# Optimization experiments

Hardware: AMD Instinct MI355X
Metric: run time of the kernel (lower is better)

Reference implementation:

```python
import jax, jax.numpy as jnp
import numpy as np

S1, S2, S3 = 2, 16, 1  # hardcoded layer sizes from __init__


def _lstm_cell(x, h, c, w_ih, w_hh, b_ih, b_hh):
    # torch.nn.LSTMCell gate order: i, f, g, o
    gates = x @ w_ih.T + b_ih + h @ w_hh.T + b_hh
    i, f, g, o = jnp.split(gates, 4, axis=-1)
    i = jax.nn.sigmoid(i)
    f = jax.nn.sigmoid(f)
    g = jnp.tanh(g)
    o = jax.nn.sigmoid(o)
    c_new = f * c + i * g
    h_new = o * jnp.tanh(c_new)
    return h_new, c_new


def setup_inputs() -> dict:
    key = jax.random.key(0)
    ks = jax.random.split(key, 16)
    B, T = 16384, 2048
    x = jax.random.normal(ks[0], (B, T * S1), dtype=jnp.float32)

    def u(k, shape, fan):
        bound = 1.0 / np.sqrt(fan)
        return jax.random.uniform(k, shape, jnp.float32, -bound, bound)

    return {
        "x": x,
        # lstm1: LSTMCell(2, 2)
        "w_ih1": u(ks[1], (4 * S1, S1), S1), "w_hh1": u(ks[2], (4 * S1, S1), S1),
        "b_ih1": u(ks[3], (4 * S1,), S1),   "b_hh1": u(ks[4], (4 * S1,), S1),
        # lstm2: LSTMCell(2, 16)
        "w_ih2": u(ks[5], (4 * S2, S1), S2), "w_hh2": u(ks[6], (4 * S2, S2), S2),
        "b_ih2": u(ks[7], (4 * S2,), S2),   "b_hh2": u(ks[8], (4 * S2,), S2),
        # lstm3: LSTMCell(16, 1)
        "w_ih3": u(ks[9], (4 * S3, S2), S3), "w_hh3": u(ks[10], (4 * S3, S3), S3),
        "b_ih3": u(ks[11], (4 * S3,), S3),  "b_hh3": u(ks[12], (4 * S3,), S3),
        # linear: Linear(1, 1)
        "w_lin": u(ks[13], (S3, S3), S3), "b_lin": u(ks[14], (S3,), S3),
    }


def reference(x, w_ih1, w_hh1, b_ih1, b_hh1,
              w_ih2, w_hh2, b_ih2, b_hh2,
              w_ih3, w_hh3, b_ih3, b_hh3,
              w_lin, b_lin):
    B = x.shape[0]
    T = x.shape[1] // S1
    # [B, T*2] -> [T, B, 2] (time-major for scan)
    xt = x.reshape(B, T, S1).transpose(1, 0, 2)

    h1 = jnp.zeros((B, S1), x.dtype); c1 = jnp.zeros((B, S1), x.dtype)
    h2 = jnp.zeros((B, S2), x.dtype); c2 = jnp.zeros((B, S2), x.dtype)
    h3 = jnp.zeros((B, S3), x.dtype); c3 = jnp.zeros((B, S3), x.dtype)

    def step(carry, x_t):
        h1, c1, h2, c2, h3, c3 = carry
        h1, c1 = _lstm_cell(x_t, h1, c1, w_ih1, w_hh1, b_ih1, b_hh1)
        h2, c2 = _lstm_cell(h1, h2, c2, w_ih2, w_hh2, b_ih2, b_hh2)
        h3, c3 = _lstm_cell(h2, h3, c3, w_ih3, w_hh3, b_ih3, b_hh3)
        out = h3 @ w_lin.T + b_lin  # [B, 1]
        return (h1, c1, h2, c2, h3, c3), out

    _, ys = jax.lax.scan(step, (h1, c1, h2, c2, h3, c3), xt)
    # ys: [T, B, 1] -> cat along dim=1 of per-step [B,1] outputs -> [B, T]
    return ys[:, :, 0].T
```

## Files before the change

kernel.cpp:

```cpp
#include <hip/hip_runtime.h>

typedef _Float16 f16x8 __attribute__((ext_vector_type(8)));
typedef float    f32x4 __attribute__((ext_vector_type(4)));
typedef unsigned u32x4 __attribute__((ext_vector_type(4)));

#define DEV __device__ __forceinline__

DEV float fexp2(float x){ return __builtin_amdgcn_exp2f(x); }
DEV float frcp (float x){ return __builtin_amdgcn_rcpf(x); }

DEV float sgm(float p){ return frcp(1.0f + fexp2(p)); }
DEV float tnc(float c){ return fmaf(2.f, sgm(c * -2.88539008177792682f), -1.f); }

DEV float shx(float v, int m){ return __shfl_xor(v, m, 64); }

DEV unsigned pkrne(float a, float b){
  unsigned short ha = __builtin_bit_cast(unsigned short, (_Float16)a);
  unsigned short hb = __builtin_bit_cast(unsigned short, (_Float16)b);
  return (unsigned)ha | ((unsigned)hb << 16);
}

#define L2E_N  (-1.44269504088896341f)
#define L2E2_N (-2.88539008177792682f)

__global__ __launch_bounds__(256, 1)
void lstm3_kernel(const float* __restrict__ x,
                  const float* __restrict__ w_ih1, const float* __restrict__ w_hh1,
                  const float* __restrict__ b_ih1, const float* __restrict__ b_hh1,
                  const float* __restrict__ w_ih2, const float* __restrict__ w_hh2,
                  const float* __restrict__ b_ih2, const float* __restrict__ b_hh2,
                  const float* __restrict__ w_ih3, const float* __restrict__ w_hh3,
                  const float* __restrict__ b_ih3, const float* __restrict__ b_hh3,
                  const float* __restrict__ w_lin, const float* __restrict__ b_lin,
                  float* __restrict__ out, int T)
{
  const int tid = threadIdx.x;
  const int l   = tid & 63;
  const int n   = l & 15;
  const int g   = l >> 4;
  const int wv  = tid >> 6;
  const int seq = 16 * (blockIdx.x * 4 + wv) + n;

  const int rA = g, rB = 4 + g;
  const float sAq = L2E_N;
  const float sBq = (g < 2) ? L2E2_N : L2E_N;
  const float m1  = (g < 2) ? 2.0f : 1.0f;
  const float a1  = (g < 2) ? -1.0f : 0.0f;
  const float w1ax = w_ih1[2*rA]*sAq,  w1ay = w_ih1[2*rA+1]*sAq;
  const float w1ah0 = w_hh1[2*rA]*sAq, w1ah1 = w_hh1[2*rA+1]*sAq;
  const float bbA  = (b_ih1[rA] + b_hh1[rA]) * sAq;
  const float w1bx = w_ih1[2*rB]*sBq,  w1by = w_ih1[2*rB+1]*sBq;
  const float w1bh0 = w_hh1[2*rB]*sBq, w1bh1 = w_hh1[2*rB+1]*sBq;
  const float bbB  = (b_ih1[rB] + b_hh1[rB]) * sBq;

  f16x8 af[4];
  f16x8 a2f[4];
  f32x4 cb[4];
  #pragma unroll
  for (int t = 0; t < 4; ++t){
    const float sc = (t == 2) ? L2E2_N : L2E_N;
    #pragma unroll
    for (int e = 0; e < 8; ++e){
      float v = 0.0f;
      if (e < 4) v = w_hh2[(16*t + n)*16 + (4*g + e)];
      af[t][e] = (_Float16)(v * sc);
      float v2 = 0.0f;
      if (g == 0 && e < 2) v2 = w_ih2[(16*t + n)*2 + e];
      a2f[t][e] = (_Float16)(v2 * sc);
    }
    #pragma unroll
    for (int j = 0; j < 4; ++j){
      const int r = 16*t + 4*g + j;
      cb[t][j] = (b_ih2[r] + b_hh2[r]) * sc;
    }
  }

  const float s3n = ((n & 3) == 2) ? L2E2_N : L2E_N;
  f16x8 a3f;
  #pragma unroll
  for (int e = 0; e < 8; ++e){
    float v = 0.0f;
    if (e < 4) v = w_ih3[16*(n & 3) + 4*g + e] * s3n;
    a3f[e] = (_Float16)v;
  }
  f32x4 c3v;
  c3v[0] = (b_ih3[0] + b_hh3[0]) * L2E_N;
  c3v[1] = (b_ih3[1] + b_hh3[1]) * L2E_N;
  c3v[2] = (b_ih3[2] + b_hh3[2]) * L2E2_N;
  c3v[3] = (b_ih3[3] + b_hh3[3]) * L2E_N;
  const float wh30 = w_hh3[0] * L2E_N,  wh31 = w_hh3[1] * L2E_N;
  const float wh32 = w_hh3[2] * L2E2_N, wh33 = w_hh3[3] * L2E_N;
  const float wl = w_lin[0], bl = b_lin[0];

  float c1 = 0.f, c3 = 0.f;
  float c2[4] = {0.f, 0.f, 0.f, 0.f};
  float h1a_all = 0.f, h1b_all = 0.f, h3 = 0.f;
  unsigned pAu = 0u, pBu = 0u;
  unsigned h1p = 0u;

  const float* xrow = x + (size_t)seq * (size_t)(2*T);
  float*       orow = out + (size_t)seq * (size_t)T;

  float2 x_use = *(const float2*)(xrow);
  float2 x_pre = *(const float2*)(xrow + 2);

  #define LSTM1_STEP(X0, X1)                                                   \
  {                                                                            \
    const float gA = fmaf(w1ax, (X0), fmaf(w1ay, (X1),                         \
                     fmaf(w1ah0, h1a_all, fmaf(w1ah1, h1b_all, bbA))));        \
    const float gB = fmaf(w1bx, (X0), fmaf(w1by, (X1),                         \
                     fmaf(w1bh0, h1a_all, fmaf(w1bh1, h1b_all, bbB))));        \
    const float zA = sgm(gA);                                                  \
    const float zB = fmaf(sgm(gB), m1, a1);                                    \
    const float ig1 = zA * zB;                                                 \
    const float fm = shx(zA, 32);                                              \
    c1 = fmaf(fm, c1, ig1);                                                    \
    const float th1 = tnc(c1);                                                 \
    const float om = shx(zB, 32);                                              \
    const float h1v = om * th1;                                                \
    const float t16 = shx(h1v, 16);                                            \
    h1p = pkrne(h1v, t16);                         \
    const float a_c = (g & 1) ? t16 : h1v;                                     \
    const float b_c = (g & 1) ? h1v : t16;                                     \
    const float a32 = shx(a_c, 32);                                            \
    const float b32 = shx(b_c, 32);                                            \
    h1a_all = (g & 2) ? a32 : a_c;                                             \
    h1b_all = (g & 2) ? b32 : b_c;                                             \
  }

  LSTM1_STEP(x_use.x, x_use.y)

  float o0 = 0.f, o1 = 0.f, o2 = 0.f, o3 = 0.f;

  f32x4 dp0, dp1, dp2, dp3;
  {
    u32x4 bu; bu[0] = 0u; bu[1] = 0u; bu[2] = 0u; bu[3] = 0u;
    const f16x8 bv = __builtin_bit_cast(f16x8, bu);
    dp0 = __builtin_amdgcn_mfma_f32_16x16x32_f16(af[0], bv, cb[0], 0, 0, 0);
    dp1 = __builtin_amdgcn_mfma_f32_16x16x32_f16(af[1], bv, cb[1], 0, 0, 0);
    dp2 = __builtin_amdgcn_mfma_f32_16x16x32_f16(af[2], bv, cb[2], 0, 0, 0);
    dp3 = __builtin_amdgcn_mfma_f32_16x16x32_f16(af[3], bv, cb[3], 0, 0, 0);
  }

  const int NCH = T / 4;
  for (int ch = 0; ch < NCH; ++ch){
    const bool cap = (g == (ch & 3));

    #pragma unroll
    for (int s = 0; s < 4; ++s){
      u32x4 b2u; b2u[0] = (g == 0) ? h1p : 0u; b2u[1] = 0u; b2u[2] = 0u; b2u[3] = 0u;
      const f16x8 b2v = __builtin_bit_cast(f16x8, b2u);
      const f32x4 d0 = __builtin_amdgcn_mfma_f32_16x16x32_f16(a2f[0], b2v, dp0, 0, 0, 0);
      const f32x4 d1 = __builtin_amdgcn_mfma_f32_16x16x32_f16(a2f[1], b2v, dp1, 0, 0, 0);
      const f32x4 d2 = __builtin_amdgcn_mfma_f32_16x16x32_f16(a2f[2], b2v, dp2, 0, 0, 0);
      const f32x4 d3 = __builtin_amdgcn_mfma_f32_16x16x32_f16(a2f[3], b2v, dp3, 0, 0, 0);

      const float2 xv = x_pre;
      const int ti = 4*ch + s + 2;
      const int tc = (ti < T) ? ti : (T - 1);
      x_pre = *(const float2*)(xrow + 2*tc);

      LSTM1_STEP(xv.x, xv.y)

      float h2l[4];
      #pragma unroll
      for (int j = 0; j < 4; ++j){
        const float ii = sgm(d0[j]);
        const float ff = sgm(d1[j]);
        const float gg = fmaf(2.f, sgm(d2[j]), -1.f);
        const float oo = sgm(d3[j]);
        c2[j] = fmaf(ff, c2[j], ii * gg);
        h2l[j] = oo * tnc(c2[j]);
      }
      pAu = pkrne(h2l[0], h2l[1]);
      pBu = pkrne(h2l[2], h2l[3]);

      u32x4 bu; bu[0] = pAu; bu[1] = pBu; bu[2] = 0u; bu[3] = 0u;
      const f16x8 bv = __builtin_bit_cast(f16x8, bu);
      dp0 = __builtin_amdgcn_mfma_f32_16x16x32_f16(af[0], bv, cb[0], 0, 0, 0);
      dp1 = __builtin_amdgcn_mfma_f32_16x16x32_f16(af[1], bv, cb[1], 0, 0, 0);
      dp2 = __builtin_amdgcn_mfma_f32_16x16x32_f16(af[2], bv, cb[2], 0, 0, 0);
      dp3 = __builtin_amdgcn_mfma_f32_16x16x32_f16(af[3], bv, cb[3], 0, 0, 0);

      const f32x4 d3v = __builtin_amdgcn_mfma_f32_16x16x32_f16(a3f, bv, c3v, 0, 0, 0);
      const float p_i = fmaf(wh30, h3, d3v[0]);
      const float p_f = fmaf(wh31, h3, d3v[1]);
      const float p_g = fmaf(wh32, h3, d3v[2]);
      const float p_o = fmaf(wh33, h3, d3v[3]);
      const float i3 = sgm(p_i);
      const float f3 = sgm(p_f);
      const float g3 = fmaf(2.f, sgm(p_g), -1.f);
      const float q3 = sgm(p_o);
      c3 = fmaf(f3, c3, i3 * g3);
      h3 = q3 * tnc(c3);
      const float yv = fmaf(wl, h3, bl);

      if      (s == 0) o0 = cap ? yv : o0;
      else if (s == 1) o1 = cap ? yv : o1;
      else if (s == 2) o2 = cap ? yv : o2;
      else             o3 = cap ? yv : o3;
    }

    if ((ch & 3) == 3){
      float4 o4; o4.x = o0; o4.y = o1; o4.z = o2; o4.w = o3;
      *(float4*)(orow + (ch >> 2) * 16 + 4 * g) = o4;
    }
  }
  #undef LSTM1_STEP
}

extern "C" void kernel_launch(void* const* d_in, const int* in_sizes, int n_in,
                              void* d_out, int out_size, void* d_ws, size_t ws_size,
                              hipStream_t stream)
{
  const float* x     = (const float*)d_in[0];
  const float* w_ih1 = (const float*)d_in[1];
  const float* w_hh1 = (const float*)d_in[2];
  const float* b_ih1 = (const float*)d_in[3];
  const float* b_hh1 = (const float*)d_in[4];
  const float* w_ih2 = (const float*)d_in[5];
  const float* w_hh2 = (const float*)d_in[6];
  const float* b_ih2 = (const float*)d_in[7];
  const float* b_hh2 = (const float*)d_in[8];
  const float* w_ih3 = (const float*)d_in[9];
  const float* w_hh3 = (const float*)d_in[10];
  const float* b_ih3 = (const float*)d_in[11];
  const float* b_hh3 = (const float*)d_in[12];
  const float* w_lin = (const float*)d_in[13];
  const float* b_lin = (const float*)d_in[14];
  float* out = (float*)d_out;

  const int T = 2048;
  const int B = in_sizes[0] / (2 * T);
  const int waves   = B / 16;
  const int blocks  = waves / 4;

  lstm3_kernel<<<blocks, 256, 0, stream>>>(
      x, w_ih1, w_hh1, b_ih1, b_hh1,
      w_ih2, w_hh2, b_ih2, b_hh2,
      w_ih3, w_hh3, b_ih3, b_hh3,
      w_lin, b_lin, out, T);
}
```

Measured before the change: 1.085 ms.

## Split LSTM layers across producer/consumer wave pairs via LDS double buffer

Each group of 16 sequences is now handled by two waves. A producer wave runs LSTM layers 1 and 2 and writes packed h2 into a double-buffered LDS slot, and a consumer wave runs layer 3 plus the linear output one step behind. This shortens each wave's serial dependency chain and doubles the wave count, with launch bounds raised so two blocks can share a CU. The cost is a __syncthreads every timestep and twice the blocks for the same batch. Which wave of the pair produces alternates with block index.

```diff
diff --git a/kernel.cpp b/kernel.cpp
--- a/kernel.cpp
+++ b/kernel.cpp
@@ -23,7 +23,7 @@
 #define L2E_N  (-1.44269504088896341f)
 #define L2E2_N (-2.88539008177792682f)
 
-__global__ __launch_bounds__(256, 1)
+__global__ __launch_bounds__(256, 2)
 void lstm3_kernel(const float* __restrict__ x,
                   const float* __restrict__ w_ih1, const float* __restrict__ w_hh1,
                   const float* __restrict__ b_ih1, const float* __restrict__ b_hh1,
@@ -34,12 +34,17 @@
                   const float* __restrict__ w_lin, const float* __restrict__ b_lin,
                   float* __restrict__ out, int T)
 {
+  __shared__ unsigned long long lbuf[2][2][64];
+
   const int tid = threadIdx.x;
   const int l   = tid & 63;
   const int n   = l & 15;
   const int g   = l >> 4;
   const int wv  = tid >> 6;
-  const int seq = 16 * (blockIdx.x * 4 + wv) + n;
+  const int pr  = wv >> 1;
+  const int par = (blockIdx.x >> 8) & 1;
+  const bool isP = ((wv & 1) == par);
+  const int seq = 16 * (blockIdx.x * 2 + pr) + n;
 
   const int rA = g, rB = 4 + g;
   const float sAq = L2E_N;
@@ -95,7 +100,6 @@
   float c1 = 0.f, c3 = 0.f;
   float c2[4] = {0.f, 0.f, 0.f, 0.f};
   float h1a_all = 0.f, h1b_all = 0.f, h3 = 0.f;
-  unsigned pAu = 0u, pBu = 0u;
   unsigned h1p = 0u;
 
   const float* xrow = x + (size_t)seq * (size_t)(2*T);
@@ -119,7 +123,7 @@
     const float om = shx(zB, 32);                                              \
     const float h1v = om * th1;                                                \
     const float t16 = shx(h1v, 16);                                            \
-    h1p = pkrne(h1v, t16);                         \
+    h1p = pkrne(h1v, t16);                                                     \
     const float a_c = (g & 1) ? t16 : h1v;                                     \
     const float b_c = (g & 1) ? h1v : t16;                                     \
     const float a32 = shx(a_c, 32);                                            \
@@ -129,8 +133,6 @@
   }
 
   LSTM1_STEP(x_use.x, x_use.y)
-
-  float o0 = 0.f, o1 = 0.f, o2 = 0.f, o3 = 0.f;
 
   f32x4 dp0, dp1, dp2, dp3;
   {
@@ -142,12 +144,10 @@
     dp3 = __builtin_amdgcn_mfma_f32_16x16x32_f16(af[3], bv, cb[3], 0, 0, 0);
   }
 
-  const int NCH = T / 4;
-  for (int ch = 0; ch < NCH; ++ch){
-    const bool cap = (g == (ch & 3));
-
-    #pragma unroll
-    for (int s = 0; s < 4; ++s){
+  float o0 = 0.f, o1 = 0.f, o2 = 0.f, o3 = 0.f;
+
+  for (int t = 0; t <= T; ++t){
+    if (isP && t < T){
       u32x4 b2u; b2u[0] = (g == 0) ? h1p : 0u; b2u[1] = 0u; b2u[2] = 0u; b2u[3] = 0u;
       const f16x8 b2v = __builtin_bit_cast(f16x8, b2u);
       const f32x4 d0 = __builtin_amdgcn_mfma_f32_16x16x32_f16(a2f[0], b2v, dp0, 0, 0, 0);
@@ -156,7 +156,7 @@
       const f32x4 d3 = __builtin_amdgcn_mfma_f32_16x16x32_f16(a2f[3], b2v, dp3, 0, 0, 0);
 
       const float2 xv = x_pre;
-      const int ti = 4*ch + s + 2;
+      const int ti = t + 2;
       const int tc = (ti < T) ? ti : (T - 1);
       x_pre = *(const float2*)(xrow + 2*tc);
 
@@ -172,8 +172,8 @@
         c2[j] = fmaf(ff, c2[j], ii * gg);
         h2l[j] = oo * tnc(c2[j]);
       }
-      pAu = pkrne(h2l[0], h2l[1]);
-      pBu = pkrne(h2l[2], h2l[3]);
+      const unsigned pAu = pkrne(h2l[0], h2l[1]);
+      const unsigned pBu = pkrne(h2l[2], h2l[3]);
 
       u32x4 bu; bu[0] = pAu; bu[1] = pBu; bu[2] = 0u; bu[3] = 0u;
       const f16x8 bv = __builtin_bit_cast(f16x8, bu);
@@ -182,6 +182,16 @@
       dp2 = __builtin_amdgcn_mfma_f32_16x16x32_f16(af[2], bv, cb[2], 0, 0, 0);
       dp3 = __builtin_amdgcn_mfma_f32_16x16x32_f16(af[3], bv, cb[3], 0, 0, 0);
 
+      lbuf[pr][t & 1][l] = ((unsigned long long)pBu << 32) | (unsigned long long)pAu;
+    }
+
+    if (!isP && t > 0){
+      const int u = t - 1;
+      const unsigned long long v = lbuf[pr][u & 1][l];
+      const unsigned pAu = (unsigned)v;
+      const unsigned pBu = (unsigned)(v >> 32);
+      u32x4 bu; bu[0] = pAu; bu[1] = pBu; bu[2] = 0u; bu[3] = 0u;
+      const f16x8 bv = __builtin_bit_cast(f16x8, bu);
       const f32x4 d3v = __builtin_amdgcn_mfma_f32_16x16x32_f16(a3f, bv, c3v, 0, 0, 0);
       const float p_i = fmaf(wh30, h3, d3v[0]);
       const float p_f = fmaf(wh31, h3, d3v[1]);
@@ -195,16 +205,21 @@
       h3 = q3 * tnc(c3);
       const float yv = fmaf(wl, h3, bl);
 
+      const int ch = u >> 2;
+      const int s  = u & 3;
+      const bool cap = (g == (ch & 3));
       if      (s == 0) o0 = cap ? yv : o0;
       else if (s == 1) o1 = cap ? yv : o1;
       else if (s == 2) o2 = cap ? yv : o2;
       else             o3 = cap ? yv : o3;
-    }
-
-    if ((ch & 3) == 3){
-      float4 o4; o4.x = o0; o4.y = o1; o4.z = o2; o4.w = o3;
-      *(float4*)(orow + (ch >> 2) * 16 + 4 * g) = o4;
-    }
+
+      if ((u & 15) == 15){
+        float4 o4; o4.x = o0; o4.y = o1; o4.z = o2; o4.w = o3;
+        *(float4*)(orow + (u >> 4) * 16 + 4 * g) = o4;
+      }
+    }
+
+    __syncthreads();
   }
   #undef LSTM1_STEP
 }
@@ -232,8 +247,7 @@
 
   const int T = 2048;
   const int B = in_sizes[0] / (2 * T);
-  const int waves   = B / 16;
-  const int blocks  = waves / 4;
+  const int blocks = B / 32;
 
   lstm3_kernel<<<blocks, 256, 0, stream>>>(
       x, w_ih1, w_hh1, b_ih1, b_hh1,
```

Result: slower. 1.500 ms (+38.2%).

## Fuse LSTM2 input and recurrent MFMAs; spread LSTM3 gates across lane groups

Applied to the files above, without the earlier changes.

The LSTM2 input-weight columns are packed into the unused K slots of the recurrent weight fragment. The gate preactivations are now one MFMA per gate block, with h2 and h1 in the B operand, rather than a precomputed recurrent MFMA plus a separate input MFMA accumulated on top. LSTM3 gate nonlinearities are split so each lane group evaluates one gate, and the results are exchanged with cross-lane shuffles instead of every lane computing all four sigmoids. This cuts MFMA count and transcendental work per step. In exchange, the LSTM2 MFMA now sits on the critical path right after h1/h2 are ready, and LSTM3 adds shuffle latency.

```diff
diff --git a/kernel.cpp b/kernel.cpp
--- a/kernel.cpp
+++ b/kernel.cpp
@@ -54,7 +54,6 @@
   const float bbB  = (b_ih1[rB] + b_hh1[rB]) * sBq;
 
   f16x8 af[4];
-  f16x8 a2f[4];
   f32x4 cb[4];
   #pragma unroll
   for (int t = 0; t < 4; ++t){
@@ -62,11 +61,9 @@
     #pragma unroll
     for (int e = 0; e < 8; ++e){
       float v = 0.0f;
-      if (e < 4) v = w_hh2[(16*t + n)*16 + (4*g + e)];
+      if (e < 4)                 v = w_hh2[(16*t + n)*16 + (4*g + e)];
+      else if (g == 0 && e < 6)  v = w_ih2[(16*t + n)*2 + (e - 4)];
       af[t][e] = (_Float16)(v * sc);
-      float v2 = 0.0f;
-      if (g == 0 && e < 2) v2 = w_ih2[(16*t + n)*2 + e];
-      a2f[t][e] = (_Float16)(v2 * sc);
     }
     #pragma unroll
     for (int j = 0; j < 4; ++j){
@@ -88,13 +85,15 @@
   c3v[1] = (b_ih3[1] + b_hh3[1]) * L2E_N;
   c3v[2] = (b_ih3[2] + b_hh3[2]) * L2E2_N;
   c3v[3] = (b_ih3[3] + b_hh3[3]) * L2E_N;
-  const float wh30 = w_hh3[0] * L2E_N,  wh31 = w_hh3[1] * L2E_N;
-  const float wh32 = w_hh3[2] * L2E2_N, wh33 = w_hh3[3] * L2E_N;
+  const float s3g  = (g == 2) ? L2E2_N : L2E_N;
+  const float m3g  = (g == 2) ? 2.0f : 1.0f;
+  const float a3g  = (g == 2) ? -1.0f : 0.0f;
+  const float wh3own = w_hh3[g] * s3g;
   const float wl = w_lin[0], bl = b_lin[0];
 
   float c1 = 0.f, c3 = 0.f;
   float c2[4] = {0.f, 0.f, 0.f, 0.f};
-  float h1a_all = 0.f, h1b_all = 0.f, h3 = 0.f;
+  float h1a_all = 0.f, h1b_all = 0.f, h3_all = 0.f;
   unsigned pAu = 0u, pBu = 0u;
   unsigned h1p = 0u;
 
@@ -132,28 +131,18 @@
 
   float o0 = 0.f, o1 = 0.f, o2 = 0.f, o3 = 0.f;
 
-  f32x4 dp0, dp1, dp2, dp3;
-  {
-    u32x4 bu; bu[0] = 0u; bu[1] = 0u; bu[2] = 0u; bu[3] = 0u;
-    const f16x8 bv = __builtin_bit_cast(f16x8, bu);
-    dp0 = __builtin_amdgcn_mfma_f32_16x16x32_f16(af[0], bv, cb[0], 0, 0, 0);
-    dp1 = __builtin_amdgcn_mfma_f32_16x16x32_f16(af[1], bv, cb[1], 0, 0, 0);
-    dp2 = __builtin_amdgcn_mfma_f32_16x16x32_f16(af[2], bv, cb[2], 0, 0, 0);
-    dp3 = __builtin_amdgcn_mfma_f32_16x16x32_f16(af[3], bv, cb[3], 0, 0, 0);
-  }
-
   const int NCH = T / 4;
   for (int ch = 0; ch < NCH; ++ch){
     const bool cap = (g == (ch & 3));
 
     #pragma unroll
     for (int s = 0; s < 4; ++s){
-      u32x4 b2u; b2u[0] = (g == 0) ? h1p : 0u; b2u[1] = 0u; b2u[2] = 0u; b2u[3] = 0u;
-      const f16x8 b2v = __builtin_bit_cast(f16x8, b2u);
-      const f32x4 d0 = __builtin_amdgcn_mfma_f32_16x16x32_f16(a2f[0], b2v, dp0, 0, 0, 0);
-      const f32x4 d1 = __builtin_amdgcn_mfma_f32_16x16x32_f16(a2f[1], b2v, dp1, 0, 0, 0);
-      const f32x4 d2 = __builtin_amdgcn_mfma_f32_16x16x32_f16(a2f[2], b2v, dp2, 0, 0, 0);
-      const f32x4 d3 = __builtin_amdgcn_mfma_f32_16x16x32_f16(a2f[3], b2v, dp3, 0, 0, 0);
+      u32x4 bu; bu[0] = pAu; bu[1] = pBu; bu[2] = (g == 0) ? h1p : 0u; bu[3] = 0u;
+      const f16x8 bv = __builtin_bit_cast(f16x8, bu);
+      const f32x4 d0 = __builtin_amdgcn_mfma_f32_16x16x32_f16(af[0], bv, cb[0], 0, 0, 0);
+      const f32x4 d1 = __builtin_amdgcn_mfma_f32_16x16x32_f16(af[1], bv, cb[1], 0, 0, 0);
+      const f32x4 d2 = __builtin_amdgcn_mfma_f32_16x16x32_f16(af[2], bv, cb[2], 0, 0, 0);
+      const f32x4 d3 = __builtin_amdgcn_mfma_f32_16x16x32_f16(af[3], bv, cb[3], 0, 0, 0);
 
       const float2 xv = x_pre;
       const int ti = 4*ch + s + 2;
@@ -175,25 +164,25 @@
       pAu = pkrne(h2l[0], h2l[1]);
       pBu = pkrne(h2l[2], h2l[3]);
 
-      u32x4 bu; bu[0] = pAu; bu[1] = pBu; bu[2] = 0u; bu[3] = 0u;
-      const f16x8 bv = __builtin_bit_cast(f16x8, bu);
-      dp0 = __builtin_amdgcn_mfma_f32_16x16x32_f16(af[0], bv, cb[0], 0, 0, 0);
-      dp1 = __builtin_amdgcn_mfma_f32_16x16x32_f16(af[1], bv, cb[1], 0, 0, 0);
-      dp2 = __builtin_amdgcn_mfma_f32_16x16x32_f16(af[2], bv, cb[2], 0, 0, 0);
-      dp3 = __builtin_amdgcn_mfma_f32_16x16x32_f16(af[3], bv, cb[3], 0, 0, 0);
-
-      const f32x4 d3v = __builtin_amdgcn_mfma_f32_16x16x32_f16(a3f, bv, c3v, 0, 0, 0);
-      const float p_i = fmaf(wh30, h3, d3v[0]);
-      const float p_f = fmaf(wh31, h3, d3v[1]);
-      const float p_g = fmaf(wh32, h3, d3v[2]);
-      const float p_o = fmaf(wh33, h3, d3v[3]);
-      const float i3 = sgm(p_i);
-      const float f3 = sgm(p_f);
-      const float g3 = fmaf(2.f, sgm(p_g), -1.f);
-      const float q3 = sgm(p_o);
-      c3 = fmaf(f3, c3, i3 * g3);
-      h3 = q3 * tnc(c3);
-      const float yv = fmaf(wl, h3, bl);
+      u32x4 b3; b3[0] = pAu; b3[1] = pBu; b3[2] = 0u; b3[3] = 0u;
+      const f16x8 b3v = __builtin_bit_cast(f16x8, b3);
+      const f32x4 d3v = __builtin_amdgcn_mfma_f32_16x16x32_f16(a3f, b3v, c3v, 0, 0, 0);
+
+      const float pg = (g == 0) ? d3v[0] : (g == 1) ? d3v[1] : (g == 2) ? d3v[2] : d3v[3];
+      const float P  = fmaf(wh3own, h3_all, pg);
+      const float z  = fmaf(sgm(P), m3g, a3g);
+      const float gv = shx(z, 32);
+      const float ig3 = z * gv;
+      const float fv = shx(z, 16);
+      c3 = fmaf(fv, c3, ig3);
+      const float th3 = tnc(c3);
+      const float ov3 = shx(gv, 16);
+      const float h3v = ov3 * th3;
+      const float u16 = shx(h3v, 16);
+      const float selh = (g & 1) ? u16 : h3v;
+      const float u32v = shx(selh, 32);
+      h3_all = (g & 2) ? u32v : selh;
+      const float yv = fmaf(wl, h3_all, bl);
 
       if      (s == 0) o0 = cap ? yv : o0;
       else if (s == 1) o1 = cap ? yv : o1;
```

New measurement: 1.227 ms. 1.13x slower.
